# Kernel tuning notes

Hardware: AMD Instinct MI355X
Metric: run time of the kernel (lower is better)

The kernel has to match this reference:

```python
import jax, jax.numpy as jnp
import numpy as np

N, F, E, C, CELL = 2048, 64, 4, 3, 15
OUT_CH, OUT_K, N_CLASS = 10, 15, 2


def _xex(X, A_attr, wx0, wx1, we):
    # pairwise score tensor: Y[i,j] = X[i]@wx0 + X[j]@wx1 + A_attr[i,j]@we -> [N,N,c_out]
    return (X @ wx0)[:, None, :] + (X @ wx1)[None, :, :] + jnp.einsum('ije,ec->ijc', A_attr, we)


def _gcn_layer(X, A, A_attr, ax0, ax1, ae, ix0, ix1, ie, gx0, gx1, ge, wr):
    n = X.shape[0]
    # multi-channel attention (MA) branch
    att = jax.nn.elu(_xex(X, A_attr, ax0, ax1, ae)) + 1.0001  # [n,n,C]
    att = att * A[:, :, None]
    att = jax.nn.softmax(att, axis=1)  # softmax over neighbor axis (incl. zeroed entries, as in TF code)
    att = att * A[:, :, None]
    y_node = jnp.einsum('ijc,jf->icf', att, X).reshape(n, -1)        # [n, C*F_in]
    y_edge = jnp.einsum('ijc,ije->ice', att, A_attr).reshape(n, -1)  # [n, C*E]
    # gated branch (unmasked sum over all j, as in aggr_neibors_gate)
    info = jnp.tanh(_xex(X, A_attr, ix0, ix1, ie))        # [n,n,CELL]
    gate = jax.nn.sigmoid(_xex(X, A_attr, gx0, gx1, ge))  # [n,n,CELL]
    y_gate = jnp.sum(info * gate, axis=1)                 # [n, CELL]
    r = jnp.concatenate([X, y_edge, y_node, y_gate], axis=1)
    return jnp.tanh(r @ wr + 0.1)


def _forward(X, A, A_attr,
             att0_x0, att0_x1, att0_e, info0_x0, info0_x1, info0_e,
             gate0_x0, gate0_x1, gate0_e, r0,
             att1_x0, att1_x1, att1_e, info1_x0, info1_x1, info1_e,
             gate1_x0, gate1_x1, gate1_e, r1,
             out_att, out_cnn, out_r):
    h0 = _gcn_layer(X, A, A_attr, att0_x0, att0_x1, att0_e,
                    info0_x0, info0_x1, info0_e, gate0_x0, gate0_x1, gate0_e, r0)
    h1 = _gcn_layer(h0, A, A_attr, att1_x0, att1_x1, att1_e,
                    info1_x0, info1_x1, info1_e, gate1_x0, gate1_x1, gate1_e, r1)
    Xc = jnp.concatenate([X, h0, h1], axis=1)       # [n, F + 2*CELL]
    att = jax.nn.softmax(Xc @ out_att, axis=0)      # node-wise attention pooling, [n, OUT_CH]
    image = att.T @ Xc                              # [OUT_CH, F + 2*CELL]
    image = jnp.tanh(image @ out_cnn + 0.1)         # [OUT_CH, OUT_K]
    logits = image.reshape(1, -1) @ out_r + 0.1
    return jax.nn.softmax(logits, axis=-1)          # [1, N_CLASS]


def setup_inputs() -> dict:
    keys = jax.random.split(jax.random.key(0), 26)
    tn = lambda k, s: jax.random.normal(k, s, jnp.float32) * 0.05  # truncated_normal init approx
    return {
        'X': jax.random.normal(keys[0], (N, F), jnp.float32),
        'A': (jax.random.uniform(keys[1], (N, N)) < 0.02).astype(jnp.float32),  # ~40 neighbors/node
        'A_attr': jax.random.normal(keys[2], (N, N, E), jnp.float32),
        'att0_x0': tn(keys[3], (F, C)), 'att0_x1': tn(keys[4], (F, C)), 'att0_e': tn(keys[5], (E, C)),
        'info0_x0': tn(keys[6], (F, CELL)), 'info0_x1': tn(keys[7], (F, CELL)), 'info0_e': tn(keys[8], (E, CELL)),
        'gate0_x0': tn(keys[9], (F, CELL)), 'gate0_x1': tn(keys[10], (F, CELL)), 'gate0_e': tn(keys[11], (E, CELL)),
        'r0': tn(keys[12], (F + (F + E) * C + CELL, CELL)),
        'att1_x0': tn(keys[13], (CELL, C)), 'att1_x1': tn(keys[14], (CELL, C)), 'att1_e': tn(keys[15], (E, C)),
        'info1_x0': tn(keys[16], (CELL, CELL)), 'info1_x1': tn(keys[17], (CELL, CELL)), 'info1_e': tn(keys[18], (E, CELL)),
        'gate1_x0': tn(keys[19], (CELL, CELL)), 'gate1_x1': tn(keys[20], (CELL, CELL)), 'gate1_e': tn(keys[21], (E, CELL)),
        'r1': tn(keys[22], (CELL + (CELL + E) * C + CELL, CELL)),
        'out_att': tn(keys[23], (F + 2 * CELL, OUT_CH)),
        'out_cnn': tn(keys[24], (F + 2 * CELL, OUT_K)),
        'out_r': tn(keys[25], (OUT_K * OUT_CH, N_CLASS)),
    }


def reference(X, A, A_attr,
              att0_x0, att0_x1, att0_e, info0_x0, info0_x1, info0_e,
              gate0_x0, gate0_x1, gate0_e, r0,
              att1_x0, att1_x1, att1_e, info1_x0, info1_x1, info1_e,
              gate1_x0, gate1_x1, gate1_e, r1,
              out_att, out_cnn, out_r):
    return _forward(X, A, A_attr,
                    att0_x0, att0_x1, att0_e, info0_x0, info0_x1, info0_e,
                    gate0_x0, gate0_x1, gate0_e, r0,
                    att1_x0, att1_x1, att1_e, info1_x0, info1_x1, info1_e,
                    gate1_x0, gate1_x1, gate1_e, r1,
                    out_att, out_cnn, out_r)
```

## Files before the change

kernel.cpp:

```cpp
#include <hip/hip_runtime.h>
#include <hip/hip_bf16.h>
#include <math.h>

#define NN 2048
#define EE 4
#define CC 3
#define CELL 15
#define MAXD 128
#define GATE_JZ 4

typedef unsigned short u16;

__device__ __forceinline__ float b2f(u16 u) { return __uint_as_float(((unsigned int)u) << 16); }
__device__ __forceinline__ u16 f2b(float f) {
    unsigned int x = __float_as_uint(f);
    unsigned int r = (x + 0x7fffu + ((x >> 16) & 1u)) >> 16;
    return (u16)r;
}
__device__ __forceinline__ float fastrcp(float x) { return __builtin_amdgcn_rcpf(x); }
__device__ __forceinline__ float fastexp2(float x) { return __builtin_amdgcn_exp2f(x); }
__device__ __forceinline__ float rfl(float x) {
    return __uint_as_float(__builtin_amdgcn_readfirstlane(__float_as_uint(x)));
}
__device__ __forceinline__ float ldx(const void* p, size_t i, bool bf) {
    if (bf) return b2f(((const u16*)p)[i]);
    return ((const float*)p)[i];
}
__device__ __forceinline__ bool detect_bf(const u16* X) {
    int lane = threadIdx.x & 63;
    u16 u = X[2 * lane];
    int e = (u >> 7) & 0xFF;
    unsigned long long m = __ballot(e >= 100 && e <= 150);
    return __popcll(m) >= 32;
}

__global__ __launch_bounds__(256) void k_edges(const void* __restrict__ A, const u16* __restrict__ Xd,
                                               int* __restrict__ flag, int* __restrict__ deg,
                                               int* __restrict__ edges) {
    bool bf = detect_bf(Xd);
    if (blockIdx.x == 0 && threadIdx.x == 0) *flag = bf ? 1 : 0;
    int lane = threadIdx.x & 63, wv = threadIdx.x >> 6;
    int i = blockIdx.x * 4 + wv;
    int base = 0;
    for (int jb = 0; jb < NN; jb += 64) {
        float a = ldx(A, (size_t)i * NN + jb + lane, bf);
        unsigned long long m = __ballot(a != 0.f);
        if (a != 0.f) {
            int slot = base + __popcll(m & ((1ull << lane) - 1ull));
            if (slot < MAXD) edges[i * MAXD + slot] = jb + lane;
        }
        base += __popcll(m);
    }
    if (lane == 0) deg[i] = base;
}

template<int FIN, bool XRAW>
__global__ void k_proj(const int* __restrict__ flag, const void* __restrict__ Xin_,
                       const void* __restrict__ ax0, const void* __restrict__ ax1,
                       const void* __restrict__ ix0, const void* __restrict__ ix1,
                       const void* __restrict__ gx0, const void* __restrict__ gx1,
                       float* __restrict__ p0, float* __restrict__ pj,
                       float* __restrict__ pa0, float* __restrict__ pa1) {
    __shared__ float xs[FIN];
    bool bf = (*flag != 0);
    bool xbf = XRAW ? bf : false;
    int nd = blockIdx.x;
    int t = threadIdx.x;
    if (t < FIN) xs[t] = ldx(Xin_, (size_t)nd * FIN + t, xbf);
    __syncthreads();
    if (t >= 66) return;
    const void* W; int col, OUT; float* dst;
    if (t < 15)      { W = ix0; col = t;      OUT = CELL; dst = p0  + nd * 30 + t; }
    else if (t < 30) { W = gx0; col = t - 15; OUT = CELL; dst = p0  + nd * 30 + t; }
    else if (t < 45) { W = ix1; col = t - 30; OUT = CELL; dst = pj  + nd * 30 + (t - 30); }
    else if (t < 60) { W = gx1; col = t - 45; OUT = CELL; dst = pj  + nd * 30 + (t - 30); }
    else if (t < 63) { W = ax0; col = t - 60; OUT = CC;   dst = pa0 + nd * 3 + (t - 60); }
    else             { W = ax1; col = t - 63; OUT = CC;   dst = pa1 + nd * 3 + (t - 63); }
    float acc = 0.f;
    for (int f = 0; f < FIN; ++f) acc += xs[f] * ldx(W, (size_t)f * OUT + col, bf);
    *dst = acc;
}

template<int FIN, bool BF, bool XRAW>
__device__ void att_body(const void* __restrict__ Xin_, const void* __restrict__ A_attr,
                         const void* __restrict__ ae,
                         const float* __restrict__ pa0, const float* __restrict__ pa1,
                         const int* __restrict__ deg, const int* __restrict__ edges,
                         float* __restrict__ y_node, float* __restrict__ y_edge,
                         float (*ew)[4], float* pdn, float* pne, float* pnn) {
    int i = blockIdx.x;
    int t = threadIdx.x;
    int lane = t & 63, wv = t >> 6;
    float aew[EE][CC];
    #pragma unroll
    for (int e = 0; e < EE; ++e)
        #pragma unroll
        for (int c = 0; c < CC; ++c) aew[e][c] = ldx(ae, e * CC + c, BF);
    float pa0v[3] = { pa0[i*3], pa0[i*3+1], pa0[i*3+2] };
    int dg = deg[i]; if (dg > MAXD) dg = MAXD;
    float dn[3] = {0.f, 0.f, 0.f};
    float ne[3][4] = {{0.f}};
    for (int base = 0; base < dg; base += 256) {
        int idx = base + t;
        if (idx < dg) {
            int j = edges[i * MAXD + idx];
            float a0, a1, a2, a3;
            if (BF) {
                const u16* ap = (const u16*)A_attr + ((size_t)i * NN + j) * EE;
                ushort4 av = *(const ushort4*)ap;
                a0 = b2f(av.x); a1 = b2f(av.y); a2 = b2f(av.z); a3 = b2f(av.w);
            } else {
                const float* ap = (const float*)A_attr + ((size_t)i * NN + j) * EE;
                float4 av = *(const float4*)ap;
                a0 = av.x; a1 = av.y; a2 = av.z; a3 = av.w;
            }
            float w[3];
            #pragma unroll
            for (int c = 0; c < 3; ++c) {
                float s = pa0v[c] + pa1[j*3 + c]
                        + a0*aew[0][c] + a1*aew[1][c] + a2*aew[2][c] + a3*aew[3][c];
                float val = (s > 0.f) ? (s + 1.0001f) : (__expf(s) - 1.f + 1.0001f);
                float wc = __expf(val);
                w[c] = wc;
                dn[c] += wc;
                ne[c][0] += wc * a0; ne[c][1] += wc * a1; ne[c][2] += wc * a2; ne[c][3] += wc * a3;
            }
            ew[idx][0] = __int_as_float(j);
            ew[idx][1] = w[0]; ew[idx][2] = w[1]; ew[idx][3] = w[2];
        }
    }
    #pragma unroll
    for (int off = 32; off; off >>= 1) {
        #pragma unroll
        for (int c = 0; c < 3; ++c) {
            dn[c] += __shfl_xor(dn[c], off);
            #pragma unroll
            for (int e = 0; e < 4; ++e) ne[c][e] += __shfl_xor(ne[c][e], off);
        }
    }
    if (lane == 0) {
        #pragma unroll
        for (int c = 0; c < 3; ++c) {
            pdn[wv*3 + c] = dn[c];
            #pragma unroll
            for (int e = 0; e < 4; ++e) pne[(wv*3 + c)*4 + e] = ne[c][e];
        }
    }
    __syncthreads();
    float rdn[3];
    #pragma unroll
    for (int c = 0; c < 3; ++c) {
        float s = (float)(NN - dg);
        #pragma unroll
        for (int w2 = 0; w2 < 4; ++w2) s += pdn[w2*3 + c];
        rdn[c] = 1.f / s;
    }
    float nn0 = 0.f, nn1 = 0.f, nn2 = 0.f;
    bool xbf = XRAW ? BF : false;
    for (int idx = wv; idx < dg; idx += 4) {
        int j = __float_as_int(ew[idx][0]);
        float w0 = ew[idx][1], w1 = ew[idx][2], w2 = ew[idx][3];
        if (lane < FIN) {
            float x = ldx(Xin_, (size_t)j * FIN + lane, xbf);
            nn0 += w0 * x; nn1 += w1 * x; nn2 += w2 * x;
        }
    }
    if (lane < FIN) {
        pnn[(wv*3 + 0)*64 + lane] = nn0;
        pnn[(wv*3 + 1)*64 + lane] = nn1;
        pnn[(wv*3 + 2)*64 + lane] = nn2;
    }
    __syncthreads();
    if (t < FIN) {
        #pragma unroll
        for (int c = 0; c < 3; ++c) {
            float s = pnn[(0*3+c)*64 + t] + pnn[(1*3+c)*64 + t]
                    + pnn[(2*3+c)*64 + t] + pnn[(3*3+c)*64 + t];
            y_node[(size_t)i * (3*FIN) + c*FIN + t] = s * rdn[c];
        }
    }
    if (t == 0) {
        #pragma unroll
        for (int c = 0; c < 3; ++c)
            #pragma unroll
            for (int e = 0; e < 4; ++e) {
                float s = pne[(0*3+c)*4+e] + pne[(1*3+c)*4+e] + pne[(2*3+c)*4+e] + pne[(3*3+c)*4+e];
                y_edge[(size_t)i * 12 + c*4 + e] = s * rdn[c];
            }
    }
}

template<int FIN, bool XRAW>
__global__ __launch_bounds__(256) void k_att(
        const int* __restrict__ flag,
        const void* __restrict__ Xin_, const void* __restrict__ A_attr, const void* __restrict__ ae,
        const float* __restrict__ pa0, const float* __restrict__ pa1,
        const int* __restrict__ deg, const int* __restrict__ edges,
        float* __restrict__ y_node, float* __restrict__ y_edge) {
    __shared__ float ew[MAXD][4];
    __shared__ float pdn[4*3];
    __shared__ float pne[4*3*4];
    __shared__ float pnn[4*3*64];
    if (*flag) att_body<FIN, true,  XRAW>(Xin_, A_attr, ae, pa0, pa1, deg, edges, y_node, y_edge, ew, pdn, pne, pnn);
    else       att_body<FIN, false, XRAW>(Xin_, A_attr, ae, pa0, pa1, deg, edges, y_node, y_edge, ew, pdn, pne, pnn);
}

template<bool BF, int K0, int NK>
__device__ void gate_half(const void* __restrict__ A_attr,
                          const void* __restrict__ iew, const void* __restrict__ gew,
                          const float* __restrict__ p0, const float* __restrict__ pj,
                          float* __restrict__ ygp, float* lds) {
    constexpr int T = 128;
    constexpr int JCH = NN / GATE_JZ;
    constexpr float L2E = 1.4426950408889634f;
    const int lane = threadIdx.x & 63;
    const int i = blockIdx.x * 4 + (threadIdx.x >> 6);
    const int jb0 = blockIdx.z * JCH;

    float Wi[EE][NK], Wg[EE][NK];
    #pragma unroll
    for (int e = 0; e < EE; ++e)
        #pragma unroll
        for (int k = 0; k < NK; ++k) {
            Wi[e][k] = rfl(ldx(iew, e*CELL + K0 + k, BF) * (-2.f * L2E));
            Wg[e][k] = rfl(ldx(gew, e*CELL + K0 + k, BF) * (-L2E));
        }
    float p0i[NK], p0g[NK];
    #pragma unroll
    for (int k = 0; k < NK; ++k) {
        p0i[k] = rfl(p0[(size_t)i*30 + K0 + k] * (-2.f * L2E));
        p0g[k] = rfl(p0[(size_t)i*30 + 15 + K0 + k] * (-L2E));
    }
    float acc[NK] = {0.f};

    for (int tb = jb0; tb < jb0 + JCH; tb += T) {
        __syncthreads();
        #pragma unroll
        for (int s = 0; s < 8; ++s) {
            int q = threadIdx.x + 256 * s;
            int r = q >> 4, c = q & 15;
            if (c < 2 * NK) {
                float scale = (c < NK) ? (-2.f * L2E) : (-L2E);
                int ksrc = (c < NK) ? (K0 + c) : (15 + K0 + (c - NK));
                lds[r * 17 + c] = pj[(size_t)(tb + r) * 30 + ksrc] * scale;
            }
        }
        __syncthreads();
        #pragma unroll
        for (int js = 0; js < T; js += 64) {
            int r = js + lane;
            int j = tb + r;
            float a0, a1, a2, a3;
            if (BF) {
                const u16* ap = (const u16*)A_attr + ((size_t)i * NN + j) * EE;
                ushort4 av = *(const ushort4*)ap;
                a0 = b2f(av.x); a1 = b2f(av.y); a2 = b2f(av.z); a3 = b2f(av.w);
            } else {
                const float* ap = (const float*)A_attr + ((size_t)i * NN + j) * EE;
                float4 av = *(const float4*)ap;
                a0 = av.x; a1 = av.y; a2 = av.z; a3 = av.w;
            }
            const float* rowp = lds + r * 17;
            float pv[2 * NK];
            #pragma unroll
            for (int c = 0; c < 2 * NK; ++c) pv[c] = rowp[c];
            #pragma unroll
            for (int k = 0; k < NK; ++k) {
                float t = p0i[k] + pv[k]      + a0*Wi[0][k] + a1*Wi[1][k] + a2*Wi[2][k] + a3*Wi[3][k];
                float u = p0g[k] + pv[NK + k] + a0*Wg[0][k] + a1*Wg[1][k] + a2*Wg[2][k] + a3*Wg[3][k];
                float e1 = fastexp2(t);
                float e2 = fastexp2(u);
                acc[k] = fmaf(1.f - e1, fastrcp((1.f + e1) * (1.f + e2)), acc[k]);
            }
        }
    }
    #pragma unroll
    for (int off = 32; off; off >>= 1)
        #pragma unroll
        for (int k = 0; k < NK; ++k) acc[k] += __shfl_xor(acc[k], off);
    if (lane == 0) {
        #pragma unroll
        for (int k = 0; k < NK; ++k)
            ygp[((size_t)blockIdx.z * NN + i) * CELL + K0 + k] = acc[k];
    }
}

__global__ __launch_bounds__(256, 2) void k_gate(
        const int* __restrict__ flag,
        const void* __restrict__ A_attr, const void* __restrict__ iew, const void* __restrict__ gew,
        const float* __restrict__ p0, const float* __restrict__ pj, float* __restrict__ ygp) {
    __shared__ float lds[128 * 17];
    if (*flag) {
        if (blockIdx.y == 0) gate_half<true, 0, 8>(A_attr, iew, gew, p0, pj, ygp, lds);
        else                 gate_half<true, 8, 7>(A_attr, iew, gew, p0, pj, ygp, lds);
    } else {
        if (blockIdx.y == 0) gate_half<false, 0, 8>(A_attr, iew, gew, p0, pj, ygp, lds);
        else                 gate_half<false, 8, 7>(A_attr, iew, gew, p0, pj, ygp, lds);
    }
}

__global__ __launch_bounds__(256) void k_hp(const int* __restrict__ flag,
        const void* __restrict__ X, const float* __restrict__ y_edge,
        const float* __restrict__ y_node, const float* __restrict__ y_gate,
        const void* __restrict__ wr,
        const void* __restrict__ ax0, const void* __restrict__ ax1,
        const void* __restrict__ ix0, const void* __restrict__ ix1,
        const void* __restrict__ gx0, const void* __restrict__ gx1,
        float* __restrict__ h0,
        float* __restrict__ p0o, float* __restrict__ pjo,
        float* __restrict__ pa0o, float* __restrict__ pa1o) {
    __shared__ float v[283];
    __shared__ float part[CELL][16];
    __shared__ float hs[CELL];
    bool bf = (*flag != 0);
    int nd = blockIdx.x, t = threadIdx.x;
    for (int q = t; q < 64; q += 256)  v[q]       = ldx(X, (size_t)nd * 64 + q, bf);
    for (int q = t; q < 12; q += 256)  v[64 + q]  = y_edge[(size_t)nd * 12 + q];
    for (int q = t; q < 192; q += 256) v[76 + q]  = y_node[(size_t)nd * 192 + q];
    for (int q = t; q < 15; q += 256) {
        float s = 0.f;
        #pragma unroll
        for (int z = 0; z < GATE_JZ; ++z) s += y_gate[((size_t)z * NN + nd) * CELL + q];
        v[268 + q] = s;
    }
    __syncthreads();
    if (t < 240) {
        int k = t >> 4, sub = t & 15;
        float acc = 0.f;
        for (int r = sub; r < 283; r += 16) acc += v[r] * ldx(wr, (size_t)r * CELL + k, bf);
        part[k][sub] = acc;
    }
    __syncthreads();
    if (t < CELL) {
        float acc = 0.1f;
        #pragma unroll
        for (int s = 0; s < 16; ++s) acc += part[t][s];
        float hv = tanhf(acc);
        hs[t] = hv;
        h0[(size_t)nd * CELL + t] = hv;
    }
    __syncthreads();
    if (t < 66) {
        const void* W; int col, OUT; float* dst;
        if (t < 15)      { W = ix0; col = t;      OUT = CELL; dst = p0o  + nd * 30 + t; }
        else if (t < 30) { W = gx0; col = t - 15; OUT = CELL; dst = p0o  + nd * 30 + t; }
        else if (t < 45) { W = ix1; col = t - 30; OUT = CELL; dst = pjo  + nd * 30 + (t - 30); }
        else if (t < 60) { W = gx1; col = t - 45; OUT = CELL; dst = pjo  + nd * 30 + (t - 30); }
        else if (t < 63) { W = ax0; col = t - 60; OUT = CC;   dst = pa0o + nd * 3 + (t - 60); }
        else             { W = ax1; col = t - 63; OUT = CC;   dst = pa1o + nd * 3 + (t - 63); }
        float acc = 0.f;
        for (int f = 0; f < CELL; ++f) acc += hs[f] * ldx(W, (size_t)f * OUT + col, bf);
        *dst = acc;
    }
}

__global__ __launch_bounds__(256) void k_hf(const int* __restrict__ flag,
        const void* __restrict__ X, const float* __restrict__ h0,
        const float* __restrict__ y_edge, const float* __restrict__ y_node,
        const float* __restrict__ y_gate, const void* __restrict__ wr,
        const void* __restrict__ oatt,
        float* __restrict__ h1, float* __restrict__ P) {
    __shared__ float v[87];
    __shared__ float xv[64];
    __shared__ float part[CELL][16];
    __shared__ float hs[CELL];
    __shared__ float pp[10][16];
    bool bf = (*flag != 0);
    int nd = blockIdx.x, t = threadIdx.x;
    for (int q = t; q < 15; q += 256) v[q]      = h0[(size_t)nd * 15 + q];
    for (int q = t; q < 12; q += 256) v[15 + q] = y_edge[(size_t)nd * 12 + q];
    for (int q = t; q < 45; q += 256) v[27 + q] = y_node[(size_t)nd * 45 + q];
    for (int q = t; q < 15; q += 256) {
        float s = 0.f;
        #pragma unroll
        for (int z = 0; z < GATE_JZ; ++z) s += y_gate[((size_t)z * NN + nd) * CELL + q];
        v[72 + q] = s;
    }
    for (int q = t; q < 64; q += 256) xv[q]     = ldx(X, (size_t)nd * 64 + q, bf);
    __syncthreads();
    if (t < 240) {
        int k = t >> 4, sub = t & 15;
        float acc = 0.f;
        for (int r = sub; r < 87; r += 16) acc += v[r] * ldx(wr, (size_t)r * CELL + k, bf);
        part[k][sub] = acc;
    }
    __syncthreads();
    if (t < CELL) {
        float acc = 0.1f;
        #pragma unroll
        for (int s = 0; s < 16; ++s) acc += part[t][s];
        float hv = tanhf(acc);
        hs[t] = hv;
        h1[(size_t)nd * CELL + t] = hv;
    }
    __syncthreads();
    if (t < 160) {
        int c = t >> 4, sub = t & 15;
        float acc = 0.f;
        for (int d = sub; d < 94; d += 16) {
            float x = (d < 64) ? xv[d] : (d < 79) ? v[d - 64] : hs[d - 79];
            acc += x * ldx(oatt, (size_t)d * 10 + c, bf);
        }
        pp[c][sub] = acc;
    }
    __syncthreads();
    if (t < 10) {
        float acc = 0.f;
        #pragma unroll
        for (int s = 0; s < 16; ++s) acc += pp[t][s];
        P[(size_t)nd * 10 + t] = acc;
    }
}

__global__ __launch_bounds__(1024) void k_f2(const float* __restrict__ P, float* __restrict__ wsm,
                                             float* __restrict__ imgp) {
    __shared__ float red[16][10];
    int t = threadIdx.x; int lane = t & 63; int wv = t >> 6;
    for (int q = t; q < 940; q += 1024) imgp[q] = 0.f;
    float mx[10], sm[10];
    #pragma unroll
    for (int c = 0; c < 10; ++c) mx[c] = -1e30f;
    for (int n = t; n < NN; n += 1024)
        #pragma unroll
        for (int c = 0; c < 10; ++c) mx[c] = fmaxf(mx[c], P[(size_t)n*10 + c]);
    #pragma unroll
    for (int off = 32; off; off >>= 1)
        #pragma unroll
        for (int c = 0; c < 10; ++c) mx[c] = fmaxf(mx[c], __shfl_xor(mx[c], off));
    if (lane == 0)
        #pragma unroll
        for (int c = 0; c < 10; ++c) red[wv][c] = mx[c];
    __syncthreads();
    #pragma unroll
    for (int c = 0; c < 10; ++c) {
        float m = red[0][c];
        for (int w2 = 1; w2 < 16; ++w2) m = fmaxf(m, red[w2][c]);
        mx[c] = m;
    }
    __syncthreads();
    #pragma unroll
    for (int c = 0; c < 10; ++c) sm[c] = 0.f;
    for (int n = t; n < NN; n += 1024)
        #pragma unroll
        for (int c = 0; c < 10; ++c) sm[c] += __expf(P[(size_t)n*10 + c] - mx[c]);
    #pragma unroll
    for (int off = 32; off; off >>= 1)
        #pragma unroll
        for (int c = 0; c < 10; ++c) sm[c] += __shfl_xor(sm[c], off);
    if (lane == 0)
        #pragma unroll
        for (int c = 0; c < 10; ++c) red[wv][c] = sm[c];
    __syncthreads();
    float rs[10];
    #pragma unroll
    for (int c = 0; c < 10; ++c) {
        float s = 0.f;
        for (int w2 = 0; w2 < 16; ++w2) s += red[w2][c];
        rs[c] = 1.f / s;
    }
    for (int n = t; n < NN; n += 1024)
        #pragma unroll
        for (int c = 0; c < 10; ++c) wsm[(size_t)n*10 + c] = __expf(P[(size_t)n*10 + c] - mx[c]) * rs[c];
}

__global__ __launch_bounds__(1024) void k_f3(const int* __restrict__ flag,
                     const void* __restrict__ X, const float* __restrict__ h0,
                     const float* __restrict__ h1, const float* __restrict__ wsm,
                     float* __restrict__ image_pre) {
    bool bf = (*flag != 0);
    int t = threadIdx.x;
    if (t >= 940) return;
    int ch = t / 94, d = t - ch * 94;
    int n0 = blockIdx.x * 32;
    float acc = 0.f;
    for (int nl = 0; nl < 32; ++nl) {
        int n = n0 + nl;
        float w = wsm[(size_t)n*10 + ch];
        float x = (d < 64) ? ldx(X, (size_t)n*64 + d, bf)
                : (d < 79) ? h0[(size_t)n*15 + (d - 64)]
                           : h1[(size_t)n*15 + (d - 79)];
        acc += w * x;
    }
    atomicAdd(&image_pre[t], acc);
}

__global__ __launch_bounds__(256) void k_f4(const int* __restrict__ flag,
                     const float* __restrict__ image_pre,
                     const void* __restrict__ out_cnn, const void* __restrict__ out_r,
                     void* __restrict__ out) {
    bool bf = (*flag != 0);
    __shared__ float ip[940];
    __shared__ float img2[150];
    __shared__ float red[8];
    int t = threadIdx.x;
    for (int q = t; q < 940; q += 256) ip[q] = image_pre[q];
    __syncthreads();
    if (t < 150) {
        int ch = t / 15, kk = t - ch * 15;
        float acc = 0.1f;
        for (int d = 0; d < 94; ++d) acc += ip[ch*94 + d] * ldx(out_cnn, (size_t)d*15 + kk, bf);
        img2[t] = tanhf(acc);
    }
    __syncthreads();
    float c0 = 0.f, c1 = 0.f;
    if (t < 150) {
        float vv = img2[t];
        c0 = vv * ldx(out_r, (size_t)t*2, bf);
        c1 = vv * ldx(out_r, (size_t)t*2 + 1, bf);
    }
    #pragma unroll
    for (int off = 32; off; off >>= 1) { c0 += __shfl_xor(c0, off); c1 += __shfl_xor(c1, off); }
    if ((t & 63) == 0) { red[(t >> 6)*2] = c0; red[(t >> 6)*2 + 1] = c1; }
    __syncthreads();
    if (t == 0) {
        float l0 = 0.1f + red[0] + red[2] + red[4] + red[6];
        float l1 = 0.1f + red[1] + red[3] + red[5] + red[7];
        float m = fmaxf(l0, l1);
        float e0 = __expf(l0 - m), e1 = __expf(l1 - m);
        float s = e0 + e1;
        float p0v = e0 / s, p1v = e1 / s;
        if (bf) { u16* o = (u16*)out; o[0] = f2b(p0v); o[1] = f2b(p1v); }
        else    { float* o = (float*)out; o[0] = p0v; o[1] = p1v; }
    }
}

extern "C" void kernel_launch(void* const* d_in, const int* in_sizes, int n_in,
                              void* d_out, int out_size, void* d_ws, size_t ws_size,
                              hipStream_t stream) {
    (void)in_sizes; (void)n_in; (void)out_size; (void)ws_size;
    const void* X      = d_in[0];
    const void* A      = d_in[1];
    const void* Aattr  = d_in[2];
    const void* a0x0 = d_in[3],  *a0x1 = d_in[4],  *a0e = d_in[5];
    const void* i0x0 = d_in[6],  *i0x1 = d_in[7],  *i0e = d_in[8];
    const void* g0x0 = d_in[9],  *g0x1 = d_in[10], *g0e = d_in[11];
    const void* r0   = d_in[12];
    const void* a1x0 = d_in[13], *a1x1 = d_in[14], *a1e = d_in[15];
    const void* i1x0 = d_in[16], *i1x1 = d_in[17], *i1e = d_in[18];
    const void* g1x0 = d_in[19], *g1x1 = d_in[20], *g1e = d_in[21];
    const void* r1   = d_in[22];
    const void* oatt = d_in[23], *ocnn = d_in[24], *orr = d_in[25];

    char* p = (char*)d_ws;
    auto alloc = [&](size_t bytes) -> void* { void* r = (void*)p; p += (bytes + 255) & ~(size_t)255; return r; };
    int*   flag   = (int*)  alloc(4);
    int*   deg    = (int*)  alloc(NN * 4);
    int*   edges  = (int*)  alloc((size_t)NN * MAXD * 4);
    float* p0_0   = (float*)alloc((size_t)NN * 30 * 4);
    float* pj_0   = (float*)alloc((size_t)NN * 30 * 4);
    float* pa0_0  = (float*)alloc((size_t)NN * 3 * 4);
    float* pa1_0  = (float*)alloc((size_t)NN * 3 * 4);
    float* p0_1   = (float*)alloc((size_t)NN * 30 * 4);
    float* pj_1   = (float*)alloc((size_t)NN * 30 * 4);
    float* pa0_1  = (float*)alloc((size_t)NN * 3 * 4);
    float* pa1_1  = (float*)alloc((size_t)NN * 3 * 4);
    float* ye0    = (float*)alloc((size_t)NN * 12 * 4);
    float* yn0    = (float*)alloc((size_t)NN * 192 * 4);
    float* yg0    = (float*)alloc((size_t)GATE_JZ * NN * CELL * 4);
    float* h0     = (float*)alloc((size_t)NN * CELL * 4);
    float* ye1    = (float*)alloc((size_t)NN * 12 * 4);
    float* yn1    = (float*)alloc((size_t)NN * 45 * 4);
    float* yg1    = (float*)alloc((size_t)GATE_JZ * NN * CELL * 4);
    float* h1     = (float*)alloc((size_t)NN * CELL * 4);
    float* P      = (float*)alloc((size_t)NN * 10 * 4);
    float* wsm    = (float*)alloc((size_t)NN * 10 * 4);
    float* imgp   = (float*)alloc(940 * 4);

    k_edges<<<NN / 4, 256, 0, stream>>>(A, (const u16*)X, flag, deg, edges);

    dim3 ggate(NN / 4, 2, GATE_JZ);

    k_proj<64, true><<<NN, 128, 0, stream>>>(flag, X, a0x0, a0x1, i0x0, i0x1, g0x0, g0x1, p0_0, pj_0, pa0_0, pa1_0);
    k_att<64, true><<<NN, 256, 0, stream>>>(flag, X, Aattr, a0e, pa0_0, pa1_0, deg, edges, yn0, ye0);
    k_gate<<<ggate, 256, 0, stream>>>(flag, Aattr, i0e, g0e, p0_0, pj_0, yg0);
    k_hp<<<NN, 256, 0, stream>>>(flag, X, ye0, yn0, yg0, r0,
                                 a1x0, a1x1, i1x0, i1x1, g1x0, g1x1,
                                 h0, p0_1, pj_1, pa0_1, pa1_1);

    k_att<15, false><<<NN, 256, 0, stream>>>(flag, h0, Aattr, a1e, pa0_1, pa1_1, deg, edges, yn1, ye1);
    k_gate<<<ggate, 256, 0, stream>>>(flag, Aattr, i1e, g1e, p0_1, pj_1, yg1);
    k_hf<<<NN, 256, 0, stream>>>(flag, X, h0, ye1, yn1, yg1, r1, oatt, h1, P);

    k_f2<<<1, 1024, 0, stream>>>(P, wsm, imgp);
    k_f3<<<64, 1024, 0, stream>>>(flag, X, h0, h1, wsm, imgp);
    k_f4<<<1, 256, 0, stream>>>(flag, imgp, ocnn, orr, d_out);
}
```

Baseline: 392.3 us.

## Merge attention and gate kernels into one launch and pack gate math into float2

```diff
diff --git a/kernel.cpp b/kernel.cpp
--- a/kernel.cpp
+++ b/kernel.cpp
@@ -10,6 +10,7 @@
 #define GATE_JZ 4
 
 typedef unsigned short u16;
+typedef float f32x2 __attribute__((ext_vector_type(2)));
 
 __device__ __forceinline__ float b2f(u16 u) { return __uint_as_float(((unsigned int)u) << 16); }
 __device__ __forceinline__ u16 f2b(float f) {
@@ -82,13 +83,12 @@
 }
 
 template<int FIN, bool BF, bool XRAW>
-__device__ void att_body(const void* __restrict__ Xin_, const void* __restrict__ A_attr,
+__device__ void att_body(int i, const void* __restrict__ Xin_, const void* __restrict__ A_attr,
                          const void* __restrict__ ae,
                          const float* __restrict__ pa0, const float* __restrict__ pa1,
                          const int* __restrict__ deg, const int* __restrict__ edges,
                          float* __restrict__ y_node, float* __restrict__ y_edge,
                          float (*ew)[4], float* pdn, float* pne, float* pnn) {
-    int i = blockIdx.x;
     int t = threadIdx.x;
     int lane = t & 63, wv = t >> 6;
     float aew[EE][CC];
@@ -190,46 +190,31 @@
     }
 }
 
-template<int FIN, bool XRAW>
-__global__ __launch_bounds__(256) void k_att(
-        const int* __restrict__ flag,
-        const void* __restrict__ Xin_, const void* __restrict__ A_attr, const void* __restrict__ ae,
-        const float* __restrict__ pa0, const float* __restrict__ pa1,
-        const int* __restrict__ deg, const int* __restrict__ edges,
-        float* __restrict__ y_node, float* __restrict__ y_edge) {
-    __shared__ float ew[MAXD][4];
-    __shared__ float pdn[4*3];
-    __shared__ float pne[4*3*4];
-    __shared__ float pnn[4*3*64];
-    if (*flag) att_body<FIN, true,  XRAW>(Xin_, A_attr, ae, pa0, pa1, deg, edges, y_node, y_edge, ew, pdn, pne, pnn);
-    else       att_body<FIN, false, XRAW>(Xin_, A_attr, ae, pa0, pa1, deg, edges, y_node, y_edge, ew, pdn, pne, pnn);
-}
-
 template<bool BF, int K0, int NK>
 __device__ void gate_half(const void* __restrict__ A_attr,
                           const void* __restrict__ iew, const void* __restrict__ gew,
                           const float* __restrict__ p0, const float* __restrict__ pj,
-                          float* __restrict__ ygp, float* lds) {
+                          float* __restrict__ ygp, float* lds, int gx, int gz) {
     constexpr int T = 128;
     constexpr int JCH = NN / GATE_JZ;
     constexpr float L2E = 1.4426950408889634f;
     const int lane = threadIdx.x & 63;
-    const int i = blockIdx.x * 4 + (threadIdx.x >> 6);
-    const int jb0 = blockIdx.z * JCH;
-
-    float Wi[EE][NK], Wg[EE][NK];
+    const int i = gx * 4 + (threadIdx.x >> 6);
+    const int jb0 = gz * JCH;
+
+    f32x2 W2[EE][NK];
     #pragma unroll
     for (int e = 0; e < EE; ++e)
         #pragma unroll
         for (int k = 0; k < NK; ++k) {
-            Wi[e][k] = rfl(ldx(iew, e*CELL + K0 + k, BF) * (-2.f * L2E));
-            Wg[e][k] = rfl(ldx(gew, e*CELL + K0 + k, BF) * (-L2E));
-        }
-    float p0i[NK], p0g[NK];
+            W2[e][k].x = rfl(ldx(iew, e*CELL + K0 + k, BF) * (-2.f * L2E));
+            W2[e][k].y = rfl(ldx(gew, e*CELL + K0 + k, BF) * (-L2E));
+        }
+    f32x2 p0p[NK];
     #pragma unroll
     for (int k = 0; k < NK; ++k) {
-        p0i[k] = rfl(p0[(size_t)i*30 + K0 + k] * (-2.f * L2E));
-        p0g[k] = rfl(p0[(size_t)i*30 + 15 + K0 + k] * (-L2E));
+        p0p[k].x = rfl(p0[(size_t)i*30 + K0 + k] * (-2.f * L2E));
+        p0p[k].y = rfl(p0[(size_t)i*30 + 15 + K0 + k] * (-L2E));
     }
     float acc[NK] = {0.f};
 
@@ -240,9 +225,10 @@
             int q = threadIdx.x + 256 * s;
             int r = q >> 4, c = q & 15;
             if (c < 2 * NK) {
-                float scale = (c < NK) ? (-2.f * L2E) : (-L2E);
-                int ksrc = (c < NK) ? (K0 + c) : (15 + K0 + (c - NK));
-                lds[r * 17 + c] = pj[(size_t)(tb + r) * 30 + ksrc] * scale;
+                int k = c >> 1, comp = c & 1;
+                float scale = comp ? (-L2E) : (-2.f * L2E);
+                int ksrc = comp ? (15 + K0 + k) : (K0 + k);
+                lds[r * 18 + c] = pj[(size_t)(tb + r) * 30 + ksrc] * scale;
             }
         }
         __syncthreads();
@@ -260,17 +246,19 @@
                 float4 av = *(const float4*)ap;
                 a0 = av.x; a1 = av.y; a2 = av.z; a3 = av.w;
             }
-            const float* rowp = lds + r * 17;
-            float pv[2 * NK];
-            #pragma unroll
-            for (int c = 0; c < 2 * NK; ++c) pv[c] = rowp[c];
+            f32x2 aa0 = {a0, a0}, aa1 = {a1, a1}, aa2 = {a2, a2}, aa3 = {a3, a3};
+            const float* rowp = lds + r * 18;
             #pragma unroll
             for (int k = 0; k < NK; ++k) {
-                float t = p0i[k] + pv[k]      + a0*Wi[0][k] + a1*Wi[1][k] + a2*Wi[2][k] + a3*Wi[3][k];
-                float u = p0g[k] + pv[NK + k] + a0*Wg[0][k] + a1*Wg[1][k] + a2*Wg[2][k] + a3*Wg[3][k];
-                float e1 = fastexp2(t);
-                float e2 = fastexp2(u);
-                acc[k] = fmaf(1.f - e1, fastrcp((1.f + e1) * (1.f + e2)), acc[k]);
+                f32x2 tu = *(const f32x2*)(rowp + 2*k) + p0p[k];
+                tu += aa0 * W2[0][k];
+                tu += aa1 * W2[1][k];
+                tu += aa2 * W2[2][k];
+                tu += aa3 * W2[3][k];
+                float e1 = fastexp2(tu.x);
+                float e2 = fastexp2(tu.y);
+                float d1 = 1.f + e1, d2 = 1.f + e2;
+                acc[k] = fmaf(1.f - e1, fastrcp(d1 * d2), acc[k]);
             }
         }
     }
@@ -281,21 +269,41 @@
     if (lane == 0) {
         #pragma unroll
         for (int k = 0; k < NK; ++k)
-            ygp[((size_t)blockIdx.z * NN + i) * CELL + K0 + k] = acc[k];
-    }
-}
-
-__global__ __launch_bounds__(256, 2) void k_gate(
+            ygp[((size_t)gz * NN + i) * CELL + K0 + k] = acc[k];
+    }
+}
+
+template<int FIN, bool XRAW>
+__global__ __launch_bounds__(256, 2) void k_ag(
         const int* __restrict__ flag,
-        const void* __restrict__ A_attr, const void* __restrict__ iew, const void* __restrict__ gew,
+        const void* __restrict__ Xin_, const void* __restrict__ A_attr, const void* __restrict__ ae,
+        const float* __restrict__ pa0, const float* __restrict__ pa1,
+        const int* __restrict__ deg, const int* __restrict__ edges,
+        float* __restrict__ y_node, float* __restrict__ y_edge,
+        const void* __restrict__ iew, const void* __restrict__ gew,
         const float* __restrict__ p0, const float* __restrict__ pj, float* __restrict__ ygp) {
-    __shared__ float lds[128 * 17];
-    if (*flag) {
-        if (blockIdx.y == 0) gate_half<true, 0, 8>(A_attr, iew, gew, p0, pj, ygp, lds);
-        else                 gate_half<true, 8, 7>(A_attr, iew, gew, p0, pj, ygp, lds);
+    __shared__ __align__(16) float smem[128 * 18];
+    bool bf = (*flag != 0);
+    int b = blockIdx.x;
+    if (b < NN) {
+        float (*ew)[4] = (float(*)[4])smem;
+        float* pdn = smem + 512;
+        float* pne = pdn + 12;
+        float* pnn = pne + 48;
+        if (bf) att_body<FIN, true,  XRAW>(b, Xin_, A_attr, ae, pa0, pa1, deg, edges, y_node, y_edge, ew, pdn, pne, pnn);
+        else    att_body<FIN, false, XRAW>(b, Xin_, A_attr, ae, pa0, pa1, deg, edges, y_node, y_edge, ew, pdn, pne, pnn);
     } else {
-        if (blockIdx.y == 0) gate_half<false, 0, 8>(A_attr, iew, gew, p0, pj, ygp, lds);
-        else                 gate_half<false, 8, 7>(A_attr, iew, gew, p0, pj, ygp, lds);
+        int g = b - NN;
+        int gx = g & 511;
+        int gy = (g >> 9) & 1;
+        int gz = g >> 10;
+        if (bf) {
+            if (gy == 0) gate_half<true, 0, 8>(A_attr, iew, gew, p0, pj, ygp, smem, gx, gz);
+            else         gate_half<true, 8, 7>(A_attr, iew, gew, p0, pj, ygp, smem, gx, gz);
+        } else {
+            if (gy == 0) gate_half<false, 0, 8>(A_attr, iew, gew, p0, pj, ygp, smem, gx, gz);
+            else         gate_half<false, 8, 7>(A_attr, iew, gew, p0, pj, ygp, smem, gx, gz);
+        }
     }
 }
 
@@ -568,17 +576,17 @@
 
     k_edges<<<NN / 4, 256, 0, stream>>>(A, (const u16*)X, flag, deg, edges);
 
-    dim3 ggate(NN / 4, 2, GATE_JZ);
+    const int NAG = NN + (NN / 4) * 2 * GATE_JZ;
 
     k_proj<64, true><<<NN, 128, 0, stream>>>(flag, X, a0x0, a0x1, i0x0, i0x1, g0x0, g0x1, p0_0, pj_0, pa0_0, pa1_0);
-    k_att<64, true><<<NN, 256, 0, stream>>>(flag, X, Aattr, a0e, pa0_0, pa1_0, deg, edges, yn0, ye0);
-    k_gate<<<ggate, 256, 0, stream>>>(flag, Aattr, i0e, g0e, p0_0, pj_0, yg0);
+    k_ag<64, true><<<NAG, 256, 0, stream>>>(flag, X, Aattr, a0e, pa0_0, pa1_0, deg, edges, yn0, ye0,
+                                            i0e, g0e, p0_0, pj_0, yg0);
     k_hp<<<NN, 256, 0, stream>>>(flag, X, ye0, yn0, yg0, r0,
                                  a1x0, a1x1, i1x0, i1x1, g1x0, g1x1,
                                  h0, p0_1, pj_1, pa0_1, pa1_1);
 
-    k_att<15, false><<<NN, 256, 0, stream>>>(flag, h0, Aattr, a1e, pa0_1, pa1_1, deg, edges, yn1, ye1);
-    k_gate<<<ggate, 256, 0, stream>>>(flag, Aattr, i1e, g1e, p0_1, pj_1, yg1);
+    k_ag<15, false><<<NAG, 256, 0, stream>>>(flag, h0, Aattr, a1e, pa0_1, pa1_1, deg, edges, yn1, ye1,
+                                             i1e, g1e, p0_1, pj_1, yg1);
     k_hf<<<NN, 256, 0, stream>>>(flag, X, h0, ye1, yn1, yg1, r1, oatt, h1, P);
 
     k_f2<<<1, 1024, 0, stream>>>(P, wsm, imgp);
```

Measured after the change: 506.1 us. 1.29x slower.
